# Kernel optimization log

Hardware: AMD Instinct MI355X
Metric: run time of the kernel (lower is better)

## Reference

```python
import math
import jax, jax.numpy as jnp
import numpy as np

N = 100000
E_RAND = 800000
IN_F, HID, OUT_F, HEADS = 128, 64, 64, 4
NOISE_SCALE = 1.0 * math.sqrt(2.0 * math.log(1.25 / 0.05))  # dp_rate=1, eps=1, del=0.05


def setup_inputs() -> dict:
    key = jax.random.key(0)
    ks = jax.random.split(key, 12)
    x = jax.random.normal(ks[0], (N, IN_F), dtype=jnp.float32)
    src_r = jax.random.randint(ks[1], (E_RAND,), 0, N, dtype=jnp.int32)
    dst_r = jax.random.randint(ks[2], (E_RAND,), 0, N, dtype=jnp.int32)
    loops = jnp.arange(N, dtype=jnp.int32)  # add_self_loop
    src = jnp.concatenate([src_r, loops])
    dst = jnp.concatenate([dst_r, loops])
    # layer 0: GATConv(in=128, out=64, heads=4)
    s0 = 1.0 / math.sqrt(IN_F)
    W0 = jax.random.normal(ks[3], (IN_F, HEADS * HID), dtype=jnp.float32) * s0
    al0 = jax.random.normal(ks[4], (HEADS, HID), dtype=jnp.float32) * 0.1
    ar0 = jax.random.normal(ks[5], (HEADS, HID), dtype=jnp.float32) * 0.1
    b0 = jnp.zeros((HEADS * HID,), dtype=jnp.float32)
    # layer 1: GATConv(in=256, out=64, heads=1)
    s1 = 1.0 / math.sqrt(HEADS * HID)
    W1 = jax.random.normal(ks[6], (HEADS * HID, OUT_F), dtype=jnp.float32) * s1
    al1 = jax.random.normal(ks[7], (1, OUT_F), dtype=jnp.float32) * 0.1
    ar1 = jax.random.normal(ks[8], (1, OUT_F), dtype=jnp.float32) * 0.1
    b1 = jnp.zeros((OUT_F,), dtype=jnp.float32)
    # DP gaussian noise added after first GAT layer (torch.normal(0,1,x.shape))
    noise = jax.random.normal(ks[9], (N, HEADS * HID), dtype=jnp.float32)
    return {"x": x, "src": src, "dst": dst, "W0": W0, "al0": al0, "ar0": ar0,
            "b0": b0, "W1": W1, "al1": al1, "ar1": ar1, "b1": b1, "noise": noise}


def gat_conv(x, src, dst, W, al, ar, b, apply_act):
    """DGL GATConv: per-edge attention, edge softmax over dst, scatter-sum."""
    H, D = al.shape
    h = (x @ W).reshape(-1, H, D)                      # [N,H,D]
    el = jnp.sum(h * al, axis=-1)                      # [N,H]
    er = jnp.sum(h * ar, axis=-1)                      # [N,H]
    e = jax.nn.leaky_relu(el[src] + er[dst], 0.2)      # [E,H]
    emax = jax.ops.segment_max(e, dst, num_segments=N) # [N,H]
    a = jnp.exp(e - emax[dst])
    denom = jax.ops.segment_sum(a, dst, num_segments=N)
    alpha = a / denom[dst]                             # [E,H] edge softmax
    msg = h[src] * alpha[:, :, None]                   # [E,H,D]
    out = jax.ops.segment_sum(msg, dst, num_segments=N) + b.reshape(1, H, D)
    if apply_act:
        out = jax.nn.leaky_relu(out, 0.01)             # F.leaky_relu default slope
    return out.reshape(-1, H * D)                      # flatten(1)


def reference(x, src, dst, W0, al0, ar0, b0, W1, al1, ar1, b1, noise):
    h = gat_conv(x, src, dst, W0, al0, ar0, b0, apply_act=True)   # [N, 256]
    h = h + NOISE_SCALE * noise                                   # DP noise after layer 0
    out = gat_conv(h, src, dst, W1, al1, ar1, b1, apply_act=False)  # [N, 64]
    return out
```

## Files before the change

### kernel.cpp

```cpp
#include <hip/hip_runtime.h>
#include <hip/hip_bf16.h>
#include <math.h>

#define IN_F 128
#define HID 64
#define HEADS 4
#define HD0 (HEADS * HID)
#define OUT_F 64
#define NOISE_SCALE 2.5372725354060904f

typedef __bf16 bf16x8 __attribute__((ext_vector_type(8)));
typedef float f32x4 __attribute__((ext_vector_type(4)));
typedef float f4 __attribute__((ext_vector_type(4)));
typedef unsigned int u4 __attribute__((ext_vector_type(4)));

__device__ __forceinline__ float bf2f(unsigned short u) {
    return __uint_as_float(((unsigned)u) << 16);
}
__device__ __forceinline__ unsigned short f2bf(float f) {
    unsigned u = __float_as_uint(f);
    u = u + 0x7fffu + ((u >> 16) & 1u);
    return (unsigned short)(u >> 16);
}

__device__ __forceinline__ void acc8(float* acc, const uint4& u, float wt) {
    acc[0] += wt * __uint_as_float(u.x << 16);
    acc[1] += wt * __uint_as_float(u.x & 0xffff0000u);
    acc[2] += wt * __uint_as_float(u.y << 16);
    acc[3] += wt * __uint_as_float(u.y & 0xffff0000u);
    acc[4] += wt * __uint_as_float(u.z << 16);
    acc[5] += wt * __uint_as_float(u.z & 0xffff0000u);
    acc[6] += wt * __uint_as_float(u.w << 16);
    acc[7] += wt * __uint_as_float(u.w & 0xffff0000u);
}

__device__ __forceinline__ uint4 pack8(const float4& a, const float4& b) {
    uint4 r;
    r.x = (unsigned)f2bf(a.x) | ((unsigned)f2bf(a.y) << 16);
    r.y = (unsigned)f2bf(a.z) | ((unsigned)f2bf(a.w) << 16);
    r.z = (unsigned)f2bf(b.x) | ((unsigned)f2bf(b.y) << 16);
    r.w = (unsigned)f2bf(b.z) | ((unsigned)f2bf(b.w) << 16);
    return r;
}

__global__ __launch_bounds__(256) void prep_kernel(
    int* __restrict__ deg, int N,
    unsigned long long* __restrict__ combo, int ntiles,
    const float* __restrict__ W0, unsigned short* __restrict__ W0t,
    const float* __restrict__ W1, unsigned short* __restrict__ W1t) {
    const int b = blockIdx.x;
    int i = b * 256 + threadIdx.x;
    if (i < N) deg[i] = 0;
    if (i < ntiles) combo[i] = 0ULL;
    if (b < (IN_F * HD0) / 256) {
        int n = i / IN_F, k = i % IN_F;
        W0t[i] = f2bf(W0[(size_t)k * HD0 + n]);
    } else if (b < (IN_F * HD0) / 256 + (HD0 * OUT_F) / 256) {
        int j = i - IN_F * HD0;
        int n = j / HD0, k = j % HD0;
        W1t[j] = f2bf(W1[(size_t)k * OUT_F + n]);
    }
}

__global__ __launch_bounds__(256) void gemm0_kernel(
    const float* __restrict__ x, const unsigned short* __restrict__ Bt,
    unsigned short* __restrict__ C, const float* __restrict__ al,
    const float* __restrict__ ar, float* __restrict__ el,
    float* __restrict__ er, int M) {
    constexpr int K = IN_F;
    constexpr int ASTR = K + 8;
    __shared__ __align__(16) unsigned short As[128 * ASTR];
    const int tid = threadIdx.x;
    const int lane = tid & 63, w = tid >> 6;
    const int row0 = blockIdx.x * 128;
    const int q = lane >> 4, c = lane & 15;
    const int r_st = tid >> 1, hh = tid & 1;
    {
        const int gr = row0 + r_st;
        const float* xp = x + (size_t)gr * K + hh * 16;
        unsigned short* ap = As + r_st * ASTR + hh * 16;
#pragma unroll
        for (int k0 = 0; k0 < K; k0 += 32) {
            uint4 av0 = make_uint4(0, 0, 0, 0), av1 = make_uint4(0, 0, 0, 0);
            if (gr < M) {
                const float4 fa = *(const float4*)(xp + k0);
                const float4 fb = *(const float4*)(xp + k0 + 4);
                const float4 fc = *(const float4*)(xp + k0 + 8);
                const float4 fd = *(const float4*)(xp + k0 + 12);
                av0 = pack8(fa, fb);
                av1 = pack8(fc, fd);
            }
            *(uint4*)(ap + k0) = av0;
            *(uint4*)(ap + k0 + 8) = av1;
        }
    }
    __syncthreads();
    f32x4 acc[2][16] = {};
#pragma unroll
    for (int k0 = 0; k0 < K; k0 += 32) {
        const bf16x8 af0 = *(const bf16x8*)(As + (w * 32 + c) * ASTR + k0 + q * 8);
        const bf16x8 af1 = *(const bf16x8*)(As + (w * 32 + 16 + c) * ASTR + k0 + q * 8);
#pragma unroll
        for (int nt = 0; nt < 16; ++nt) {
            const bf16x8 bfr =
                *(const bf16x8*)(Bt + (size_t)(nt * 16 + c) * K + k0 + q * 8);
            acc[0][nt] = __builtin_amdgcn_mfma_f32_16x16x32_bf16(
                af0, bfr, acc[0][nt], 0, 0, 0);
            acc[1][nt] = __builtin_amdgcn_mfma_f32_16x16x32_bf16(
                af1, bfr, acc[1][nt], 0, 0, 0);
        }
    }
    float alv[16], arv[16];
#pragma unroll
    for (int nt = 0; nt < 16; ++nt) {
        alv[nt] = al[nt * 16 + c];
        arv[nt] = ar[nt * 16 + c];
    }
#pragma unroll
    for (int mt = 0; mt < 2; ++mt) {
#pragma unroll
        for (int r = 0; r < 4; ++r) {
            const int grow = row0 + w * 32 + mt * 16 + q * 4 + r;
            const bool ok = grow < M;
#pragma unroll
            for (int g = 0; g < 4; ++g) {
                float elp = 0.f, erp = 0.f;
#pragma unroll
                for (int t = 0; t < 4; ++t) {
                    int nt = g * 4 + t;
                    float v = acc[mt][nt][r];
                    elp += v * alv[nt];
                    erp += v * arv[nt];
                    if (ok) C[(size_t)grow * HD0 + nt * 16 + c] = f2bf(v);
                }
#pragma unroll
                for (int o = 8; o > 0; o >>= 1) {
                    elp += __shfl_down(elp, o, 16);
                    erp += __shfl_down(erp, o, 16);
                }
                if (c == 0 && ok) {
                    el[(size_t)grow * HEADS + g] = elp;
                    er[(size_t)grow * HEADS + g] = erp;
                }
            }
        }
    }
}

template <int K, int H, int NT, bool CVT>
__global__ __launch_bounds__(256) void gemm_fused_kernel(
    const void* __restrict__ Asrc, const unsigned short* __restrict__ Bt,
    unsigned short* __restrict__ C, const float* __restrict__ al,
    const float* __restrict__ ar, float* __restrict__ el,
    float* __restrict__ er, int M, int NC) {
    constexpr int BSTR = K + 8;
    constexpr int ASTR = 40;
    constexpr int NROWS = 64 * NT;
    constexpr int CSTR = NROWS + 8;
    __shared__ __align__(16) unsigned short Bs[NROWS * BSTR];
    __shared__ __align__(16) unsigned short As[128 * ASTR];
    const unsigned short* Ab = (const unsigned short*)Asrc;
    const float* Af = (const float*)Asrc;
    const int tid = threadIdx.x;
    const int lane = tid & 63, w = tid >> 6;
    const int row0 = blockIdx.y * 128;
    const int n0 = blockIdx.x * NROWS;
    for (int i = tid; i < NROWS * (K / 8); i += 256) {
        int n = i / (K / 8), kc = i % (K / 8);
        *(uint4*)(Bs + n * BSTR + kc * 8) =
            *(const uint4*)(Bt + (size_t)(n0 + n) * K + kc * 8);
    }
    f32x4 acc[2][4 * NT] = {};
    const int q = lane >> 4, c = lane & 15;
    const int r_st = tid >> 1, hh = tid & 1;
    for (int k0 = 0; k0 < K; k0 += 32) {
        int gr = row0 + r_st;
        uint4 av0 = make_uint4(0, 0, 0, 0), av1 = make_uint4(0, 0, 0, 0);
        if (gr < M) {
            if (CVT) {
                const float* xp = Af + (size_t)gr * K + k0 + hh * 16;
                const float4 fa = *(const float4*)xp;
                const float4 fb = *(const float4*)(xp + 4);
                const float4 fc = *(const float4*)(xp + 8);
                const float4 fd = *(const float4*)(xp + 12);
                av0 = pack8(fa, fb);
                av1 = pack8(fc, fd);
            } else {
                const unsigned short* ap = Ab + (size_t)gr * K + k0 + hh * 16;
                av0 = *(const uint4*)(ap);
                av1 = *(const uint4*)(ap + 8);
            }
        }
        __syncthreads();
        *(uint4*)(As + r_st * ASTR + hh * 16) = av0;
        *(uint4*)(As + r_st * ASTR + hh * 16 + 8) = av1;
        __syncthreads();
        bf16x8 af[2], bfr[4 * NT];
        af[0] = *(const bf16x8*)(As + (w * 32 + c) * ASTR + q * 8);
        af[1] = *(const bf16x8*)(As + (w * 32 + 16 + c) * ASTR + q * 8);
#pragma unroll
        for (int nt = 0; nt < 4 * NT; ++nt)
            bfr[nt] = *(const bf16x8*)(Bs + (nt * 16 + c) * BSTR + k0 + q * 8);
#pragma unroll
        for (int mt = 0; mt < 2; ++mt)
#pragma unroll
            for (int nt = 0; nt < 4 * NT; ++nt)
                acc[mt][nt] = __builtin_amdgcn_mfma_f32_16x16x32_bf16(
                    af[mt], bfr[nt], acc[mt][nt], 0, 0, 0);
    }
    float alv[4 * NT], arv[4 * NT];
#pragma unroll
    for (int nt = 0; nt < 4 * NT; ++nt) {
        alv[nt] = al[n0 + nt * 16 + c];
        arv[nt] = ar[n0 + nt * 16 + c];
    }
    __syncthreads();
    unsigned short* Cs = Bs;
    const int headbase = n0 >> 6;
#pragma unroll
    for (int mt = 0; mt < 2; ++mt) {
#pragma unroll
        for (int r = 0; r < 4; ++r) {
            const int row = w * 32 + mt * 16 + q * 4 + r;
            const int grow = row0 + row;
            const bool ok = grow < M;
#pragma unroll
            for (int g = 0; g < NT; ++g) {
                float elp = 0.f, erp = 0.f;
#pragma unroll
                for (int t = 0; t < 4; ++t) {
                    int nt = g * 4 + t;
                    float v = acc[mt][nt][r];
                    elp += v * alv[nt];
                    erp += v * arv[nt];
                    Cs[row * CSTR + nt * 16 + c] = f2bf(v);
                }
#pragma unroll
                for (int o = 8; o > 0; o >>= 1) {
                    elp += __shfl_down(elp, o, 16);
                    erp += __shfl_down(erp, o, 16);
                }
                if (c == 0 && ok) {
                    el[(size_t)grow * H + headbase + g] = elp;
                    er[(size_t)grow * H + headbase + g] = erp;
                }
            }
        }
    }
    __syncthreads();
    constexpr int CPR = NROWS / 8;
    for (int i = tid; i < 128 * CPR; i += 256) {
        int row = i / CPR, ch = i % CPR;
        int grow = row0 + row;
        if (grow < M)
            *(uint4*)(C + (size_t)grow * NC + n0 + ch * 8) =
                *(const uint4*)(Cs + row * CSTR + ch * 8);
    }
}

__global__ __launch_bounds__(256) void degree_kernel(
    const int* __restrict__ dst, int* __restrict__ deg, int E) {
    int e = blockIdx.x * 256 + threadIdx.x;
    if (e < E) atomicAdd(&deg[dst[e]], 1);
}

__global__ __launch_bounds__(256) void scan_fused_kernel(
    const int* __restrict__ deg, int* __restrict__ off, int* __restrict__ cur,
    unsigned long long* __restrict__ combo, int N, int E) {
    const int t = blockIdx.x;
    __shared__ int s[256];
    __shared__ int sbase;
    const int tid = threadIdx.x;
    const int i = t * 256 + tid;
    const int v = (i < N) ? deg[i] : 0;
    s[tid] = v;
    __syncthreads();
    for (int d = 1; d < 256; d <<= 1) {
        int tt = (tid >= d) ? s[tid - d] : 0;
        __syncthreads();
        s[tid] += tt;
        __syncthreads();
    }
    const int tilesum = s[255];
    if (tid == 0) {
        if (t == 0) {
            atomicExch(&combo[0], (2ULL << 32) | (unsigned)tilesum);
            sbase = 0;
        } else {
            atomicExch(&combo[t], (1ULL << 32) | (unsigned)tilesum);
            int run = 0;
            int j = t - 1;
            while (true) {
                unsigned long long c;
                do {
                    c = atomicAdd(&combo[j], 0ULL);
                } while ((c >> 32) == 0ULL);
                run += (int)(c & 0xffffffffULL);
                if ((c >> 32) == 2ULL) break;
                --j;
            }
            sbase = run;
            atomicExch(&combo[t], (2ULL << 32) | (unsigned)(run + tilesum));
        }
    }
    __syncthreads();
    const int base = sbase;
    if (i < N) {
        int o = base + s[tid] - v;
        off[i] = o;
        cur[i] = o;
    }
    if (i == 0) off[N] = E;
}

__global__ __launch_bounds__(256) void fill_csr_kernel(
    const int* __restrict__ src, const int* __restrict__ dst,
    int* __restrict__ cur, int* __restrict__ csr_src, int E) {
    int e = blockIdx.x * 256 + threadIdx.x;
    if (e >= E) return;
    int d = dst[e];
    int pos = atomicAdd(&cur[d], 1);
    csr_src[pos] = src[e];
}

__global__ __launch_bounds__(256) void agg0_kernel(
    const int* __restrict__ off, const int* __restrict__ csr_src,
    const unsigned short* __restrict__ h,
    const float* __restrict__ el,
    const float* __restrict__ er,
    const float* __restrict__ b0, const float* __restrict__ noise,
    unsigned short* __restrict__ out, int N) {
    int gt = blockIdx.x * 256 + threadIdx.x;
    int n = gt >> 5;
    if (n >= N) return;
    const int lane = gt & 31;
    const int hd = lane >> 3;
    const int f0 = lane << 3;
    const float ern = er[(size_t)n * 4 + hd];
    const int beg = off[n];
    const int last = off[n + 1] - 1;
    float acc[8] = {0.f, 0.f, 0.f, 0.f, 0.f, 0.f, 0.f, 0.f};
    float l = 0.f;
    for (int p = beg; p <= last; p += 4) {
        int i1 = p + 1, i2 = p + 2, i3 = p + 3;
        const bool v1 = i1 <= last, v2 = i2 <= last, v3 = i3 <= last;
        i1 = v1 ? i1 : last;
        i2 = v2 ? i2 : last;
        i3 = v3 ? i3 : last;
        const int s0 = csr_src[p],  s1 = csr_src[i1];
        const int s2 = csr_src[i2], s3 = csr_src[i3];
        float e0 = el[(size_t)s0 * 4 + hd] + ern;
        float e1 = el[(size_t)s1 * 4 + hd] + ern;
        float e2 = el[(size_t)s2 * 4 + hd] + ern;
        float e3 = el[(size_t)s3 * 4 + hd] + ern;
        const uint4 u0 = *(const uint4*)(h + (size_t)s0 * HD0 + f0);
        const uint4 u1 = *(const uint4*)(h + (size_t)s1 * HD0 + f0);
        const uint4 u2 = *(const uint4*)(h + (size_t)s2 * HD0 + f0);
        const uint4 u3 = *(const uint4*)(h + (size_t)s3 * HD0 + f0);
        e0 = e0 > 0.f ? e0 : 0.2f * e0;
        e1 = e1 > 0.f ? e1 : 0.2f * e1;
        e2 = e2 > 0.f ? e2 : 0.2f * e2;
        e3 = e3 > 0.f ? e3 : 0.2f * e3;
        const float w0 = __expf(e0);
        const float w1 = v1 ? __expf(e1) : 0.f;
        const float w2 = v2 ? __expf(e2) : 0.f;
        const float w3 = v3 ? __expf(e3) : 0.f;
        acc8(acc, u0, w0);
        acc8(acc, u1, w1);
        acc8(acc, u2, w2);
        acc8(acc, u3, w3);
        l += (w0 + w1) + (w2 + w3);
    }
    const float rd = 1.f / l;
    const float4 ba = *(const float4*)(b0 + f0);
    const float4 bb = *(const float4*)(b0 + f0 + 4);
    const f4 na = __builtin_nontemporal_load((const f4*)(noise + (size_t)n * HD0 + f0));
    const f4 nb = __builtin_nontemporal_load((const f4*)(noise + (size_t)n * HD0 + f0 + 4));
    float o[8];
    o[0] = acc[0] * rd + ba.x;
    o[1] = acc[1] * rd + ba.y;
    o[2] = acc[2] * rd + ba.z;
    o[3] = acc[3] * rd + ba.w;
    o[4] = acc[4] * rd + bb.x;
    o[5] = acc[5] * rd + bb.y;
    o[6] = acc[6] * rd + bb.z;
    o[7] = acc[7] * rd + bb.w;
#pragma unroll
    for (int j = 0; j < 8; ++j) o[j] = o[j] > 0.f ? o[j] : 0.01f * o[j];
    o[0] += NOISE_SCALE * na.x;
    o[1] += NOISE_SCALE * na.y;
    o[2] += NOISE_SCALE * na.z;
    o[3] += NOISE_SCALE * na.w;
    o[4] += NOISE_SCALE * nb.x;
    o[5] += NOISE_SCALE * nb.y;
    o[6] += NOISE_SCALE * nb.z;
    o[7] += NOISE_SCALE * nb.w;
    uint4 ov;
    ov.x = (unsigned)f2bf(o[0]) | ((unsigned)f2bf(o[1]) << 16);
    ov.y = (unsigned)f2bf(o[2]) | ((unsigned)f2bf(o[3]) << 16);
    ov.z = (unsigned)f2bf(o[4]) | ((unsigned)f2bf(o[5]) << 16);
    ov.w = (unsigned)f2bf(o[6]) | ((unsigned)f2bf(o[7]) << 16);
    *(uint4*)(out + (size_t)n * HD0 + f0) = ov;
}

__global__ __launch_bounds__(256) void agg1_kernel(
    const int* __restrict__ off, const int* __restrict__ csr_src,
    const unsigned short* __restrict__ h,
    const float* __restrict__ el,
    const float* __restrict__ er,
    const float* __restrict__ b1, float* __restrict__ out, int N) {
    int gt = blockIdx.x * 256 + threadIdx.x;
    int n = gt >> 4;
    if (n >= N) return;
    const int lane = gt & 15;
    const int f0 = lane << 2;
    const float ern = er[n];
    const int beg = off[n];
    const int last = off[n + 1] - 1;
    float a0 = 0.f, a1 = 0.f, a2 = 0.f, a3 = 0.f, l = 0.f;
    for (int p = beg; p <= last; p += 4) {
        int i1 = p + 1, i2 = p + 2, i3 = p + 3;
        const bool v1 = i1 <= last, v2 = i2 <= last, v3 = i3 <= last;
        i1 = v1 ? i1 : last;
        i2 = v2 ? i2 : last;
        i3 = v3 ? i3 : last;
        const int s0 = csr_src[p],  s1 = csr_src[i1];
        const int s2 = csr_src[i2], s3 = csr_src[i3];
        float e0 = el[s0] + ern;
        float e1 = el[s1] + ern;
        float e2 = el[s2] + ern;
        float e3 = el[s3] + ern;
        const ushort4 u0 = *(const ushort4*)(h + (size_t)s0 * 64 + f0);
        const ushort4 u1 = *(const ushort4*)(h + (size_t)s1 * 64 + f0);
        const ushort4 u2 = *(const ushort4*)(h + (size_t)s2 * 64 + f0);
        const ushort4 u3 = *(const ushort4*)(h + (size_t)s3 * 64 + f0);
        e0 = e0 > 0.f ? e0 : 0.2f * e0;
        e1 = e1 > 0.f ? e1 : 0.2f * e1;
        e2 = e2 > 0.f ? e2 : 0.2f * e2;
        e3 = e3 > 0.f ? e3 : 0.2f * e3;
        const float w0 = __expf(e0);
        const float w1 = v1 ? __expf(e1) : 0.f;
        const float w2 = v2 ? __expf(e2) : 0.f;
        const float w3 = v3 ? __expf(e3) : 0.f;
        a0 += w0 * bf2f(u0.x) + w1 * bf2f(u1.x) + w2 * bf2f(u2.x) + w3 * bf2f(u3.x);
        a1 += w0 * bf2f(u0.y) + w1 * bf2f(u1.y) + w2 * bf2f(u2.y) + w3 * bf2f(u3.y);
        a2 += w0 * bf2f(u0.z) + w1 * bf2f(u1.z) + w2 * bf2f(u2.z) + w3 * bf2f(u3.z);
        a3 += w0 * bf2f(u0.w) + w1 * bf2f(u1.w) + w2 * bf2f(u2.w) + w3 * bf2f(u3.w);
        l += (w0 + w1) + (w2 + w3);
    }
    const float rd = 1.f / l;
    const float4 bv = *(const float4*)(b1 + f0);
    float4 o;
    o.x = a0 * rd + bv.x;
    o.y = a1 * rd + bv.y;
    o.z = a2 * rd + bv.z;
    o.w = a3 * rd + bv.w;
    *(float4*)(out + (size_t)n * 64 + f0) = o;
}

extern "C" void kernel_launch(void* const* d_in, const int* in_sizes, int n_in,
                              void* d_out, int out_size, void* d_ws, size_t ws_size,
                              hipStream_t stream) {
    const float* x     = (const float*)d_in[0];
    const int*   src   = (const int*)d_in[1];
    const int*   dst   = (const int*)d_in[2];
    const float* W0    = (const float*)d_in[3];
    const float* al0   = (const float*)d_in[4];
    const float* ar0   = (const float*)d_in[5];
    const float* b0    = (const float*)d_in[6];
    const float* W1    = (const float*)d_in[7];
    const float* al1   = (const float*)d_in[8];
    const float* ar1   = (const float*)d_in[9];
    const float* b1    = (const float*)d_in[10];
    const float* noise = (const float*)d_in[11];

    const int N = in_sizes[0] / IN_F;
    const int E = in_sizes[1];
    const int NB = (N + 255) / 256;

    char* p = (char*)d_ws;
    unsigned short* h0     = (unsigned short*)p; p += (size_t)N * HD0 * 2;
    unsigned short* agg0b  = (unsigned short*)p; p += (size_t)N * HD0 * 2;
    unsigned short* h1     = (unsigned short*)p; p += (size_t)N * OUT_F * 2;
    unsigned short* W0t    = (unsigned short*)p; p += (size_t)IN_F * HD0 * 2;
    unsigned short* W1t    = (unsigned short*)p; p += (size_t)HD0 * OUT_F * 2;
    float* el     = (float*)p; p += (size_t)N * HEADS * 4;
    float* er     = (float*)p; p += (size_t)N * HEADS * 4;
    int* deg    = (int*)p; p += (size_t)N * 4;
    int* cur    = (int*)p; p += (size_t)N * 4;
    int* off    = (int*)p; p += ((size_t)N + 4) * 4;
    unsigned long long* combo = (unsigned long long*)p; p += 512 * 8;
    int* csr_src= (int*)p; p += (size_t)E * 4;

    prep_kernel<<<NB, 256, 0, stream>>>(deg, N, combo, NB, W0, W0t, W1, W1t);

    degree_kernel<<<(E + 255) / 256, 256, 0, stream>>>(dst, deg, E);
    scan_fused_kernel<<<NB, 256, 0, stream>>>(deg, off, cur, combo, N, E);
    fill_csr_kernel<<<(E + 255) / 256, 256, 0, stream>>>(src, dst, cur, csr_src, E);

    const int MB = (N + 127) / 128;

    gemm0_kernel<<<MB, 256, 0, stream>>>(x, W0t, h0, al0, ar0, el, er, N);

    agg0_kernel<<<(unsigned)(((size_t)N * 32 + 255) / 256), 256, 0, stream>>>(
        off, csr_src, h0, el, er, b0, noise, agg0b, N);

    {
        dim3 grid(OUT_F / 64, MB);
        gemm_fused_kernel<HD0, 1, 1, false><<<grid, 256, 0, stream>>>(
            (const void*)agg0b, W1t, h1, al1, ar1, el, er, N, OUT_F);
    }

    agg1_kernel<<<(unsigned)(((size_t)N * 16 + 255) / 256), 256, 0, stream>>>(
        off, csr_src, h1, el, er, b1, (float*)d_out, N);
}
```

Before: 475.8 us.

## Split layer-0 GEMM per head with LDS-staged weights and coalesced output stores

The layer-0 GEMM now launches a 2D grid with one block column per attention head, so each block computes a 128x64 tile instead of 128x256. The head's weight slice is staged in LDS instead of being read from global memory inside the MFMA loop. The bf16 results go through LDS so they can be written to global memory as coalesced 16-byte stores, replacing scattered 2-byte stores. This cuts accumulator register pressure and raises occupancy, but each x row is now converted and loaded four times. The odd LDS strides (134, 66) also leave the 16-byte LDS accesses misaligned.

```diff
diff --git a/kernel.cpp b/kernel.cpp
--- a/kernel.cpp
+++ b/kernel.cpp
@@ -68,14 +68,19 @@
     const float* __restrict__ ar, float* __restrict__ el,
     float* __restrict__ er, int M) {
     constexpr int K = IN_F;
-    constexpr int ASTR = K + 8;
+    constexpr int ASTR = 134;
+    constexpr int BSTR = 134;
+    constexpr int CSTR = 66;
     __shared__ __align__(16) unsigned short As[128 * ASTR];
+    __shared__ __align__(16) unsigned short Bs[64 * BSTR];
     const int tid = threadIdx.x;
     const int lane = tid & 63, w = tid >> 6;
-    const int row0 = blockIdx.x * 128;
     const int q = lane >> 4, c = lane & 15;
-    const int r_st = tid >> 1, hh = tid & 1;
+    const int row0 = blockIdx.y * 128;
+    const int n0 = blockIdx.x * 64;
+    const int head = blockIdx.x;
     {
+        const int r_st = tid >> 1, hh = tid & 1;
         const int gr = row0 + r_st;
         const float* xp = x + (size_t)gr * K + hh * 16;
         unsigned short* ap = As + r_st * ASTR + hh * 16;
@@ -94,56 +99,67 @@
             *(uint4*)(ap + k0 + 8) = av1;
         }
     }
-    __syncthreads();
-    f32x4 acc[2][16] = {};
+    for (int i = tid; i < 64 * 16; i += 256) {
+        int n = i >> 4, kc = i & 15;
+        *(uint4*)(Bs + n * BSTR + kc * 8) =
+            *(const uint4*)(Bt + (size_t)(n0 + n) * K + kc * 8);
+    }
+    __syncthreads();
+    f32x4 acc[2][4] = {};
 #pragma unroll
     for (int k0 = 0; k0 < K; k0 += 32) {
         const bf16x8 af0 = *(const bf16x8*)(As + (w * 32 + c) * ASTR + k0 + q * 8);
         const bf16x8 af1 = *(const bf16x8*)(As + (w * 32 + 16 + c) * ASTR + k0 + q * 8);
 #pragma unroll
-        for (int nt = 0; nt < 16; ++nt) {
-            const bf16x8 bfr =
-                *(const bf16x8*)(Bt + (size_t)(nt * 16 + c) * K + k0 + q * 8);
+        for (int nt = 0; nt < 4; ++nt) {
+            const bf16x8 bfr = *(const bf16x8*)(Bs + (nt * 16 + c) * BSTR + k0 + q * 8);
             acc[0][nt] = __builtin_amdgcn_mfma_f32_16x16x32_bf16(
                 af0, bfr, acc[0][nt], 0, 0, 0);
             acc[1][nt] = __builtin_amdgcn_mfma_f32_16x16x32_bf16(
                 af1, bfr, acc[1][nt], 0, 0, 0);
         }
     }
-    float alv[16], arv[16];
-#pragma unroll
-    for (int nt = 0; nt < 16; ++nt) {
-        alv[nt] = al[nt * 16 + c];
-        arv[nt] = ar[nt * 16 + c];
-    }
+    float alv[4], arv[4];
+#pragma unroll
+    for (int nt = 0; nt < 4; ++nt) {
+        alv[nt] = al[n0 + nt * 16 + c];
+        arv[nt] = ar[n0 + nt * 16 + c];
+    }
+    __syncthreads();
+    unsigned short* Cs = Bs;
 #pragma unroll
     for (int mt = 0; mt < 2; ++mt) {
 #pragma unroll
         for (int r = 0; r < 4; ++r) {
-            const int grow = row0 + w * 32 + mt * 16 + q * 4 + r;
+            const int row = w * 32 + mt * 16 + q * 4 + r;
+            const int grow = row0 + row;
             const bool ok = grow < M;
-#pragma unroll
-            for (int g = 0; g < 4; ++g) {
-                float elp = 0.f, erp = 0.f;
-#pragma unroll
-                for (int t = 0; t < 4; ++t) {
-                    int nt = g * 4 + t;
-                    float v = acc[mt][nt][r];
-                    elp += v * alv[nt];
-                    erp += v * arv[nt];
-                    if (ok) C[(size_t)grow * HD0 + nt * 16 + c] = f2bf(v);
-                }
-#pragma unroll
-                for (int o = 8; o > 0; o >>= 1) {
-                    elp += __shfl_down(elp, o, 16);
-                    erp += __shfl_down(erp, o, 16);
-                }
-                if (c == 0 && ok) {
-                    el[(size_t)grow * HEADS + g] = elp;
-                    er[(size_t)grow * HEADS + g] = erp;
-                }
+            float elp = 0.f, erp = 0.f;
+#pragma unroll
+            for (int nt = 0; nt < 4; ++nt) {
+                float v = acc[mt][nt][r];
+                elp += v * alv[nt];
+                erp += v * arv[nt];
+                Cs[row * CSTR + nt * 16 + c] = f2bf(v);
+            }
+#pragma unroll
+            for (int o = 8; o > 0; o >>= 1) {
+                elp += __shfl_down(elp, o, 16);
+                erp += __shfl_down(erp, o, 16);
+            }
+            if (c == 0 && ok) {
+                el[(size_t)grow * HEADS + head] = elp;
+                er[(size_t)grow * HEADS + head] = erp;
             }
         }
+    }
+    __syncthreads();
+    for (int i = tid; i < 128 * 8; i += 256) {
+        int row = i >> 3, ch = i & 7;
+        int grow = row0 + row;
+        if (grow < M)
+            *(uint4*)(C + (size_t)grow * HD0 + n0 + ch * 8) =
+                *(const uint4*)(Cs + row * CSTR + ch * 8);
     }
 }
 
@@ -500,7 +516,10 @@
 
     const int MB = (N + 127) / 128;
 
-    gemm0_kernel<<<MB, 256, 0, stream>>>(x, W0t, h0, al0, ar0, el, er, N);
+    {
+        dim3 grid(HD0 / 64, MB);
+        gemm0_kernel<<<grid, 256, 0, stream>>>(x, W0t, h0, al0, ar0, el, er, N);
+    }
 
     agg0_kernel<<<(unsigned)(((size_t)N * 32 + 255) / 256), 256, 0, stream>>>(
         off, csr_src, h0, el, er, b0, noise, agg0b, N);
```

Result: faster. 457.8 us (-3.8%).
